# Performance work log

Measured on AMD Instinct MI355X. Metric: run time of the kernel, lower is better.

## Reference

```python
import jax, jax.numpy as jnp
import numpy as np

B, N, C, H = 4, 2048, 1024, 16
D = C // H  # dim_per_head = 64
NEG = -1e9  # stands in for -inf masked_fill (finite to keep grads clean)


def setup_inputs() -> dict:
    key0 = jax.random.key(0)
    ks = jax.random.split(key0, 12)
    inp = {
        "query": jax.random.normal(ks[0], (B, N, C), dtype=jnp.float32),
        "key": jax.random.normal(ks[1], (B, N, C), dtype=jnp.float32),
        "value": jax.random.normal(ks[2], (B, N, C), dtype=jnp.float32),
        "ratio": jax.random.uniform(ks[3], (B, N), dtype=jnp.float32),
        "attn_mask": jax.random.randint(ks[4], (B, N, N), 0, 2) == 1,
        # learned params (Linear layers are bias-free; weights stored as [in, out])
        "Wq": jax.random.normal(ks[5], (C, C), dtype=jnp.float32) / np.sqrt(C),
        "Wk": jax.random.normal(ks[6], (C, C), dtype=jnp.float32) / np.sqrt(C),
        "Wv": jax.random.normal(ks[7], (C, C), dtype=jnp.float32) / np.sqrt(C),
        "Wo": jax.random.normal(ks[8], (C, C), dtype=jnp.float32) / np.sqrt(C),
        "gamma": jnp.ones((C,), dtype=jnp.float32),
        "beta": jnp.zeros((C,), dtype=jnp.float32),
    }
    return inp


def reference(query, key, value, ratio, attn_mask, Wq, Wk, Wv, Wo, gamma, beta):
    residual = query
    # projections -> [B, H, N, D]
    q = (query @ Wq).reshape(B, N, H, D).transpose(0, 2, 1, 3)
    k = (key @ Wk).reshape(B, N, H, D).transpose(0, 2, 1, 3)
    v = (value @ Wv).reshape(B, N, H, D).transpose(0, 2, 1, 3)

    scale = D ** (-0.5)
    scores = jnp.einsum("bhid,bhjd->bhij", q, k) * scale  # [B,H,N1,N2]
    scores = jnp.where(attn_mask[:, None, :, :], NEG, scores)
    scores = scores * ratio[:, None, None, :]  # ratio broadcast over heads & queries
    # NON-STANDARD: softmax over dim=2 (the QUERY axis), faithful to source
    attn = jax.nn.softmax(scores, axis=2)
    # dropout omitted (eval mode)
    ctx = jnp.einsum("bhij,bhjd->bhid", attn, v)  # [B,H,N1,D]
    ctx = ctx.transpose(0, 2, 1, 3).reshape(B, N, C)
    out = ctx @ Wo
    x = residual + out
    # LayerNorm over last dim
    mu = jnp.mean(x, axis=-1, keepdims=True)
    var = jnp.var(x, axis=-1, keepdims=True)
    xn = (x - mu) * jax.lax.rsqrt(var + 1e-5)
    return xn * gamma + beta
```

## Files before the change

### kernel.cpp

```cpp
#include <hip/hip_runtime.h>
#include <hip/hip_bf16.h>
#include <stdint.h>

#define BB 4
#define NN 2048
#define CC 1024
#define HH 16
#define DD 64

typedef __attribute__((ext_vector_type(8))) short bf16x8;
typedef __attribute__((ext_vector_type(4))) float f32x4;

#define LOG2E 1.44269504088896f

__device__ __forceinline__ unsigned short f2bf(float x) {
  uint32_t u = __float_as_uint(x);
  uint32_t r = (u + 0x7FFFu + ((u >> 16) & 1u)) >> 16;
  return (unsigned short)r;
}
__device__ __forceinline__ float bf2f(unsigned short v) {
  return __uint_as_float(((uint32_t)v) << 16);
}
__device__ __forceinline__ float load_in_f(const void* p, size_t idx, int f32in) {
  if (f32in) return ((const float*)p)[idx];
  return bf2f(((const uint16_t*)p)[idx]);
}
__device__ __forceinline__ void gload16(uint16_t* lds_base, const uint16_t* gsrc) {
  __builtin_amdgcn_global_load_lds(
      (const __attribute__((address_space(1))) uint32_t*)(const void*)gsrc,
      (__attribute__((address_space(3))) uint32_t*)(void*)lds_base,
      16, 0, 0);
}

__global__ void detect_kernel(const uint32_t* __restrict__ q,
                              const uint32_t* __restrict__ m,
                              int* __restrict__ flags) {
  if (threadIdx.x == 0 && blockIdx.x == 0) {
    int sane = 0;
    for (int i = 0; i < 128; ++i) {
      uint32_t w = q[i];
      int e0 = (int)((w >> 7) & 0xFFu);
      int e1 = (int)((w >> 23) & 0xFFu);
      sane += (e0 >= 0x70 && e0 <= 0x8F) ? 1 : 0;
      sane += (e1 >= 0x70 && e1 <= 0x8F) ? 1 : 0;
    }
    flags[0] = (sane >= 208) ? 0 : 1;
    int allsmall = 1;
    for (int i = 0; i < 16; ++i) if (m[i] > 1u) allsmall = 0;
    flags[1] = allsmall;
  }
}

__global__ void conv_bf16_3(const void* __restrict__ s0, const void* __restrict__ s1,
                            const void* __restrict__ s2,
                            uint16_t* __restrict__ d0, uint16_t* __restrict__ d1,
                            uint16_t* __restrict__ d2,
                            int n, const int* __restrict__ flags) {
  const int f32in = flags[0];
  const void* src = (blockIdx.z == 0) ? s0 : (blockIdx.z == 1) ? s1 : s2;
  uint16_t* dst = (blockIdx.z == 0) ? d0 : (blockIdx.z == 1) ? d1 : d2;
  int idx = blockIdx.x * blockDim.x + threadIdx.x;
  const int total = n >> 2;
  const int stride = gridDim.x * blockDim.x;
  if (f32in) {
    const float4* s = (const float4*)src;
    for (; idx < total; idx += stride) {
      float4 v = s[idx];
      ushort4 o;
      o.x = f2bf(v.x); o.y = f2bf(v.y); o.z = f2bf(v.z); o.w = f2bf(v.w);
      ((ushort4*)dst)[idx] = o;
    }
  } else {
    const ushort4* s = (const ushort4*)src;
    for (; idx < total; idx += stride) ((ushort4*)dst)[idx] = s[idx];
  }
}

__global__ void conv_ratio2(const void* __restrict__ src, float* __restrict__ rs,
                            float* __restrict__ ng, int n, const int* __restrict__ flags) {
  const int f32in = flags[0];
  int idx = blockIdx.x * blockDim.x + threadIdx.x;
  const int stride = gridDim.x * blockDim.x;
  for (; idx < n; idx += stride) {
    float r = load_in_f(src, idx, f32in);
    rs[idx] = r * 0.125f * LOG2E;
    ng[idx] = r * (-1e9f) * LOG2E;
  }
}

__global__ void conv_maskbits(const void* __restrict__ src, uint32_t* __restrict__ dst,
                              int n, const int* __restrict__ flags) {
  const int isint = flags[1];
  const int gw = (blockIdx.x * blockDim.x + threadIdx.x) >> 6;
  const int lane = threadIdx.x & 63;
  const int nw = (gridDim.x * blockDim.x) >> 6;
  const int totalw = n >> 6;
  for (int w = gw; w < totalw; w += nw) {
    int e = w * 64 + lane;
    bool m;
    if (isint) m = (((const int*)src)[e] != 0);
    else       m = (((const uint8_t*)src)[e] != 0);
    unsigned long long bal = __ballot(m);
    if (lane == 0) ((unsigned long long*)dst)[w] = bal;
  }
}

__global__ __launch_bounds__(256)
void transW(const void* w0, const void* w1, const void* w2, const void* w3,
            uint16_t* __restrict__ wt, const int* __restrict__ flags) {
  const int f32in = flags[0];
  const void* src = (blockIdx.z == 0) ? w0 : (blockIdx.z == 1) ? w1
                   : (blockIdx.z == 2) ? w2 : w3;
  uint16_t* dst = wt + (size_t)blockIdx.z * CC * CC;
  __shared__ float t[32][33];
  const int tx = threadIdx.x, ty = threadIdx.y;
  const int n0 = blockIdx.x * 32, k0 = blockIdx.y * 32;
#pragma unroll
  for (int r = 0; r < 4; ++r) {
    int k = k0 + ty + r * 8;
    t[ty + r * 8][tx] = load_in_f(src, (size_t)k * CC + n0 + tx, f32in);
  }
  __syncthreads();
#pragma unroll
  for (int r = 0; r < 4; ++r) {
    int n = n0 + ty + r * 8;
    dst[(size_t)n * CC + k0 + tx] = f2bf(t[tx][ty + r * 8]);
  }
}

template <int MODE>
__global__ __launch_bounds__(256, 2)
void gemm128(const uint16_t* __restrict__ A, const uint16_t* __restrict__ Bt,
             void* __restrict__ out, const void* __restrict__ resid,
             const float* __restrict__ rowscale, const int* __restrict__ flags) {
  __shared__ uint16_t As[128 * 32];
  __shared__ uint16_t Bs[128 * 32];
  const int tid = threadIdx.x;
  const int wid = tid >> 6, lane = tid & 63;
  const int g = lane >> 4, c = lane & 15;
  const int m0 = blockIdx.x * 128, n0 = blockIdx.y * 128;
  const int wr = wid >> 1, wc = wid & 1;
  f32x4 acc[4][4] = {};
  for (int k0 = 0; k0 < 1024; k0 += 32) {
    __syncthreads();
#pragma unroll
    for (int is = 0; is < 2; ++is) {
      int sb = is * 256 + wid * 64;
      int s = sb + lane;
      int r = s >> 2, kp = s & 3;
      int kps = kp ^ ((r >> 1) & 3);
      gload16(&As[sb * 8], A + (size_t)(m0 + r) * 1024 + k0 + kps * 8);
      gload16(&Bs[sb * 8], Bt + (size_t)(n0 + r) * 1024 + k0 + kps * 8);
    }
    __syncthreads();
    bf16x8 a[4], b[4];
#pragma unroll
    for (int mi = 0; mi < 4; ++mi) {
      int row = wr * 64 + mi * 16 + c;
      a[mi] = *(const bf16x8*)&As[row * 32 + (g ^ ((row >> 1) & 3)) * 8];
    }
#pragma unroll
    for (int ni = 0; ni < 4; ++ni) {
      int row = wc * 64 + ni * 16 + c;
      b[ni] = *(const bf16x8*)&Bs[row * 32 + (g ^ ((row >> 1) & 3)) * 8];
    }
#pragma unroll
    for (int mi = 0; mi < 4; ++mi)
#pragma unroll
      for (int ni = 0; ni < 4; ++ni)
        acc[mi][ni] = __builtin_amdgcn_mfma_f32_16x16x32_bf16(a[mi], b[ni], acc[mi][ni], 0, 0, 0);
  }
  const int f32in = flags[0];
  float rsv[4][4];
  if (MODE == 0 && rowscale) {
#pragma unroll
    for (int mi = 0; mi < 4; ++mi)
#pragma unroll
      for (int r = 0; r < 4; ++r)
        rsv[mi][r] = rowscale[m0 + wr * 64 + mi * 16 + g * 4 + r];
  }
#pragma unroll
  for (int mi = 0; mi < 4; ++mi)
#pragma unroll
    for (int ni = 0; ni < 4; ++ni)
#pragma unroll
      for (int r = 0; r < 4; ++r) {
        int mrow = m0 + wr * 64 + mi * 16 + g * 4 + r;
        int ncol = n0 + wc * 64 + ni * 16 + c;
        float v = acc[mi][ni][r];
        if (MODE == 0) {
          if (rowscale) v *= rsv[mi][r];
          int b_ = mrow >> 11, i = mrow & 2047, h = ncol >> 6, d = ncol & 63;
          ((uint16_t*)out)[((size_t)(b_ * 16 + h) * 2048 + i) * 64 + d] = f2bf(v);
        } else if (MODE == 1) {
          int b_ = mrow >> 11, i = mrow & 2047, h = ncol >> 6, d = ncol & 63;
          ((uint16_t*)out)[((size_t)(b_ * 16 + h) * 64 + d) * 2048 + i] = f2bf(v);
        } else {
          size_t idx = (size_t)mrow * 1024 + ncol;
          ((float*)out)[idx] = v + load_in_f(resid, idx, f32in);
        }
      }
}

__global__ __launch_bounds__(256, 2)
void attn_stats(const uint16_t* __restrict__ qb, const uint16_t* __restrict__ kb,
                uint16_t* __restrict__ vt, const uint32_t* __restrict__ mbits,
                const float* __restrict__ ngbuf) {
  __shared__ float redL[4][128];
  __shared__ float invsh[128];
  const int tid = threadIdx.x, wid = tid >> 6, lane = tid & 63;
  const int g = lane >> 4, c = lane & 15;
  const int bh = blockIdx.x, b_ = bh >> 4;
  const int j0 = blockIdx.y * 128;
  const uint16_t* Kg = kb + (size_t)bh * NN * DD + (size_t)j0 * DD;
  const uint16_t* Qg = qb + (size_t)bh * NN * DD;
  const uint32_t* Mrow = mbits + (size_t)b_ * NN * 64 + (j0 >> 5);
  bf16x8 kf[2][8];
#pragma unroll
  for (int ks = 0; ks < 2; ++ks)
#pragma unroll
    for (int nj = 0; nj < 8; ++nj)
      kf[ks][nj] = *(const bf16x8*)(Kg + (size_t)(nj * 16 + c) * 64 + ks * 32 + g * 8);
  float ng8[8], l_[8];
#pragma unroll
  for (int nj = 0; nj < 8; ++nj) {
    ng8[nj] = ngbuf[b_ * NN + j0 + nj * 16 + c];
    l_[nj] = 0.f;
  }
  bf16x8 qa[2][2], qn[2][2];
  uint4 mqa[8], mqb[8];
#pragma unroll
  for (int ks = 0; ks < 2; ++ks)
#pragma unroll
    for (int mi = 0; mi < 2; ++mi)
      qa[ks][mi] = *(const bf16x8*)(Qg + (size_t)(wid * 32 + mi * 16 + c) * 64 + ks * 32 + g * 8);
#pragma unroll
  for (int u = 0; u < 8; ++u) {
    int mi = u >> 2, r = u & 3;
    mqa[u] = *(const uint4*)(Mrow + (size_t)(wid * 32 + mi * 16 + g * 4 + r) * 64);
  }

  auto body = [&](bf16x8 (&qc)[2][2], bf16x8 (&qp)[2][2],
                  uint4 (&mc)[8], uint4 (&mn)[8], int i0) {
    f32x4 sacc[2][8] = {};
    __builtin_amdgcn_s_setprio(1);
#pragma unroll
    for (int ks = 0; ks < 2; ++ks)
#pragma unroll
      for (int mi = 0; mi < 2; ++mi)
#pragma unroll
        for (int nj = 0; nj < 8; ++nj)
          sacc[mi][nj] = __builtin_amdgcn_mfma_f32_16x16x32_bf16(qc[ks][mi], kf[ks][nj], sacc[mi][nj], 0, 0, 0);
    __builtin_amdgcn_s_setprio(0);
    int ip = (i0 + 128) & (NN - 1);
#pragma unroll
    for (int ks = 0; ks < 2; ++ks)
#pragma unroll
      for (int mi = 0; mi < 2; ++mi)
        qp[ks][mi] = *(const bf16x8*)(Qg + (size_t)(ip + wid * 32 + mi * 16 + c) * 64 + ks * 32 + g * 8);
#pragma unroll
    for (int u = 0; u < 8; ++u) {
      int mi = u >> 2, r = u & 3;
      mn[u] = *(const uint4*)(Mrow + (size_t)(ip + wid * 32 + mi * 16 + g * 4 + r) * 64);
    }
#pragma unroll
    for (int mi = 0; mi < 2; ++mi)
#pragma unroll
      for (int r = 0; r < 4; ++r) {
        const uint4 mw = mc[mi * 4 + r];
#pragma unroll
        for (int nj = 0; nj < 8; ++nj) {
          uint32_t w = (nj < 2) ? mw.x : (nj < 4) ? mw.y : (nj < 6) ? mw.z : mw.w;
          bool bit = (w >> ((nj & 1) * 16 + c)) & 1u;
          float se = bit ? ng8[nj] : sacc[mi][nj][r];
          l_[nj] += exp2f(se);
        }
      }
  };
  for (int it = 0; it < 8; ++it) {
    body(qa, qn, mqa, mqb, it * 256);
    body(qn, qa, mqb, mqa, it * 256 + 128);
  }
#pragma unroll
  for (int nj = 0; nj < 8; ++nj) {
    float l = l_[nj];
    l += __shfl_xor(l, 16);
    l += __shfl_xor(l, 32);
    if (g == 0) redL[wid][nj * 16 + c] = l;
  }
  __syncthreads();
  if (tid < 128) {
    float L = redL[0][tid] + redL[1][tid] + redL[2][tid] + redL[3][tid];
    invsh[tid] = 1.0f / L;
  }
  __syncthreads();
  {
    const int d = tid >> 2, jseg = (tid & 3) * 32;
    uint16_t* vrow = vt + (size_t)bh * DD * NN + (size_t)d * NN + j0 + jseg;
#pragma unroll
    for (int u = 0; u < 4; ++u) {
      bf16x8 v = *(const bf16x8*)(vrow + u * 8);
      bf16x8 o;
#pragma unroll
      for (int e = 0; e < 8; ++e) {
        float f = bf2f((unsigned short)v[e]) * invsh[jseg + u * 8 + e];
        o[e] = (short)f2bf(f);
      }
      *(bf16x8*)(vrow + u * 8) = o;
    }
  }
}

__global__ __launch_bounds__(256, 3)
void attn_pv(const uint16_t* __restrict__ qb, const uint16_t* __restrict__ kb,
             const uint16_t* __restrict__ vt, const uint32_t* __restrict__ mbits,
             const float* __restrict__ ngbuf, uint16_t* __restrict__ ctxr) {
  __shared__ uint16_t Ks[2][64 * 64];
  __shared__ uint16_t Vs[2][64 * 64];
  __shared__ uint16_t Ps[128 * 64];
  const int tid = threadIdx.x, wid = tid >> 6, lane = tid & 63;
  const int g = lane >> 4, c = lane & 15;
  const int bh = blockIdx.x, b_ = bh >> 4, h = bh & 15;
  const int i0 = blockIdx.y * 128;
  const uint16_t* Qg = qb + (size_t)bh * NN * DD;
  const uint16_t* Kg = kb + (size_t)bh * NN * DD;
  const uint16_t* Vg = vt + (size_t)bh * DD * NN;
  const uint32_t* Mb = mbits + (size_t)b_ * NN * 64;
  const float* ngb = ngbuf + b_ * NN;

  auto stageK = [&](int buf, int j0) {
#pragma unroll
    for (int is = 0; is < 2; ++is) {
      int sb = is * 256 + wid * 64;
      int s = sb + lane;
      int row = s >> 3, gr = s & 7;
      gload16(&Ks[buf][sb * 8], Kg + (size_t)(j0 + row) * 64 + (gr ^ (row & 7)) * 8);
    }
  };
  auto stageV = [&](int buf, int j0) {
#pragma unroll
    for (int is = 0; is < 2; ++is) {
      int sb = is * 256 + wid * 64;
      int s = sb + lane;
      int d = s >> 3, gr = s & 7;
      gload16(&Vs[buf][sb * 8], Vg + (size_t)d * NN + j0 + (gr ^ (d & 7)) * 8);
    }
  };

  bf16x8 qf[2][2];
#pragma unroll
  for (int ks = 0; ks < 2; ++ks)
#pragma unroll
    for (int mi = 0; mi < 2; ++mi)
      qf[ks][mi] = *(const bf16x8*)(Qg + (size_t)(i0 + wid * 32 + mi * 16 + c) * 64 + ks * 32 + g * 8);

  stageK(0, 0); stageV(0, 0);
  __syncthreads();

  f32x4 cacc[2][4] = {};
  for (int t = 0; t < 32; ++t) {
    const int j0 = t * 64, cb = t & 1, nb = cb ^ 1;
    if (t < 31) { stageK(nb, j0 + 64); stageV(nb, j0 + 64); }
    uint2 mw0 = *(const uint2*)(Mb + (size_t)(i0 + wid * 32 + c) * 64 + (j0 >> 5));
    uint2 mw1 = *(const uint2*)(Mb + (size_t)(i0 + wid * 32 + 16 + c) * 64 + (j0 >> 5));
    float4 ngv[4];
#pragma unroll
    for (int nj = 0; nj < 4; ++nj)
      ngv[nj] = *(const float4*)(ngb + j0 + nj * 16 + g * 4);
    f32x4 st[4][2] = {};
    __builtin_amdgcn_s_setprio(1);
#pragma unroll
    for (int ks = 0; ks < 2; ++ks) {
      bf16x8 kfr[4];
#pragma unroll
      for (int nj = 0; nj < 4; ++nj) {
        int row = nj * 16 + c;
        kfr[nj] = *(const bf16x8*)&Ks[cb][row * 64 + (((ks * 4 + g) ^ (c & 7))) * 8];
      }
#pragma unroll
      for (int nj = 0; nj < 4; ++nj)
#pragma unroll
        for (int mi = 0; mi < 2; ++mi)
          st[nj][mi] = __builtin_amdgcn_mfma_f32_16x16x32_bf16(kfr[nj], qf[ks][mi], st[nj][mi], 0, 0, 0);
    }
    __builtin_amdgcn_s_setprio(0);
    uint2 pkv[4][2];
#pragma unroll
    for (int nj = 0; nj < 4; ++nj) {
      const float4 ngq = ngv[nj];
      float nz[4] = {ngq.x, ngq.y, ngq.z, ngq.w};
#pragma unroll
      for (int mi = 0; mi < 2; ++mi) {
        const uint2 mw = mi ? mw1 : mw0;
        uint32_t w = (nj < 2) ? mw.x : mw.y;
        float p[4];
#pragma unroll
        for (int u = 0; u < 4; ++u) {
          bool bit = (w >> ((nj & 1) * 16 + g * 4 + u)) & 1u;
          float se = bit ? nz[u] : st[nj][mi][u];
          p[u] = exp2f(se);
        }
        uint32_t lo, hi;
        asm("v_cvt_pk_bf16_f32 %0, %1, %2" : "=v"(lo) : "v"(p[0]), "v"(p[1]));
        asm("v_cvt_pk_bf16_f32 %0, %1, %2" : "=v"(hi) : "v"(p[2]), "v"(p[3]));
        pkv[nj][mi] = make_uint2(lo, hi);
      }
    }
#pragma unroll
    for (int nj = 0; nj < 4; ++nj)
#pragma unroll
      for (int mi = 0; mi < 2; ++mi) {
        int iL = wid * 32 + mi * 16 + c;
        int gran = (nj * 2 + (g >> 1)) ^ (c & 7);
        *(uint2*)((char*)Ps + iL * 128 + gran * 16 + (g & 1) * 8) = pkv[nj][mi];
      }
    __syncthreads();
    __builtin_amdgcn_s_setprio(1);
#pragma unroll
    for (int ks = 0; ks < 2; ++ks) {
      bf16x8 pa[2], vb[4];
#pragma unroll
      for (int mi = 0; mi < 2; ++mi) {
        int row = wid * 32 + mi * 16 + c;
        pa[mi] = *(const bf16x8*)((const char*)Ps + row * 128 + (((ks * 4 + g) ^ (c & 7))) * 16);
      }
#pragma unroll
      for (int nd = 0; nd < 4; ++nd) {
        int row = nd * 16 + c;
        vb[nd] = *(const bf16x8*)&Vs[cb][row * 64 + (((ks * 4 + g) ^ (c & 7))) * 8];
      }
#pragma unroll
      for (int mi = 0; mi < 2; ++mi)
#pragma unroll
        for (int nd = 0; nd < 4; ++nd)
          cacc[mi][nd] = __builtin_amdgcn_mfma_f32_16x16x32_bf16(pa[mi], vb[nd], cacc[mi][nd], 0, 0, 0);
    }
    __builtin_amdgcn_s_setprio(0);
    __syncthreads();
  }
#pragma unroll
  for (int mi = 0; mi < 2; ++mi)
#pragma unroll
    for (int nd = 0; nd < 4; ++nd)
#pragma unroll
      for (int r = 0; r < 4; ++r) {
        int i = i0 + wid * 32 + mi * 16 + g * 4 + r;
        int d = nd * 16 + c;
        ctxr[((size_t)(b_ * NN + i)) * CC + h * DD + d] = f2bf(cacc[mi][nd][r]);
      }
}

__global__ __launch_bounds__(256)
void ln_kernel(const float* __restrict__ xbuf, const void* __restrict__ gamma,
               const void* __restrict__ beta, float* __restrict__ out,
               const int* __restrict__ flags) {
  const int row = blockIdx.x;
  const int tid = threadIdx.x;
  const float4 v = ((const float4*)(xbuf + (size_t)row * CC))[tid];
  float s = v.x + v.y + v.z + v.w;
  float s2 = v.x * v.x + v.y * v.y + v.z * v.z + v.w * v.w;
#pragma unroll
  for (int off = 32; off >= 1; off >>= 1) {
    s += __shfl_xor(s, off);
    s2 += __shfl_xor(s2, off);
  }
  __shared__ float red[8];
  const int wid = tid >> 6, lane = tid & 63;
  if (lane == 0) { red[wid] = s; red[4 + wid] = s2; }
  __syncthreads();
  float ts = red[0] + red[1] + red[2] + red[3];
  float ts2 = red[4] + red[5] + red[6] + red[7];
  float mu = ts * (1.f / 1024.f);
  float var = ts2 * (1.f / 1024.f) - mu * mu;
  float rs = rsqrtf(var + 1e-5f);
  const int f32in = flags[0];
  const int cbase = tid * 4;
  float4 o;
  o.x = (v.x - mu) * rs * load_in_f(gamma, cbase + 0, f32in) + load_in_f(beta, cbase + 0, f32in);
  o.y = (v.y - mu) * rs * load_in_f(gamma, cbase + 1, f32in) + load_in_f(beta, cbase + 1, f32in);
  o.z = (v.z - mu) * rs * load_in_f(gamma, cbase + 2, f32in) + load_in_f(beta, cbase + 2, f32in);
  o.w = (v.w - mu) * rs * load_in_f(gamma, cbase + 3, f32in) + load_in_f(beta, cbase + 3, f32in);
  ((float4*)(out + (size_t)row * CC))[tid] = o;
}

extern "C" void kernel_launch(void* const* d_in, const int* in_sizes, int n_in,
                              void* d_out, int out_size, void* d_ws, size_t ws_size,
                              hipStream_t stream) {
  (void)in_sizes; (void)n_in; (void)out_size; (void)ws_size;
  char* ws = (char*)d_ws;
  size_t off = 0;
  auto alloc = [&](size_t bytes) -> void* {
    void* p = ws + off;
    off += (bytes + 255) & ~(size_t)255;
    return p;
  };
  int*      flags   = (int*)alloc(256);
  float*    rsbuf   = (float*)alloc((size_t)BB * NN * 4);
  float*    ngbuf   = (float*)alloc((size_t)BB * NN * 4);
  uint32_t* mbits   = (uint32_t*)alloc((size_t)BB * NN * 64 * 4);
  uint16_t* xq      = (uint16_t*)alloc((size_t)BB * NN * CC * 2);
  uint16_t* xk      = (uint16_t*)alloc((size_t)BB * NN * CC * 2);
  uint16_t* xv      = (uint16_t*)alloc((size_t)BB * NN * CC * 2);
  uint16_t* qb      = (uint16_t*)alloc((size_t)BB * NN * CC * 2);
  uint16_t* kb      = (uint16_t*)alloc((size_t)BB * NN * CC * 2);
  uint16_t* vtb     = (uint16_t*)alloc((size_t)BB * NN * CC * 2);
  uint16_t* Wt      = (uint16_t*)alloc((size_t)4 * CC * CC * 2);
  uint16_t* ctxr    = xq;
  float*    xbuf    = (float*)xk;

  detect_kernel<<<1, 64, 0, stream>>>((const uint32_t*)d_in[0], (const uint32_t*)d_in[4], flags);
  conv_bf16_3<<<dim3(2048, 1, 3), 256, 0, stream>>>(d_in[0], d_in[1], d_in[2],
                                                    xq, xk, xv, BB * NN * CC, flags);
  conv_ratio2<<<32, 256, 0, stream>>>(d_in[3], rsbuf, ngbuf, BB * NN, flags);
  conv_maskbits<<<2048, 256, 0, stream>>>(d_in[4], mbits, BB * NN * NN, flags);
  transW<<<dim3(32, 32, 4), dim3(32, 8), 0, stream>>>(d_in[5], d_in[6], d_in[7], d_in[8], Wt, flags);

  gemm128<0><<<dim3(64, 8), 256, 0, stream>>>(xq, Wt,               qb,  nullptr, nullptr, flags);
  gemm128<0><<<dim3(64, 8), 256, 0, stream>>>(xk, Wt + 1 * CC * CC, kb,  nullptr, rsbuf,  flags);
  gemm128<1><<<dim3(64, 8), 256, 0, stream>>>(xv, Wt + 2 * CC * CC, vtb, nullptr, nullptr, flags);

  attn_stats<<<dim3(64, 16), 256, 0, stream>>>(qb, kb, vtb, mbits, ngbuf);
  attn_pv<<<dim3(64, 16), 256, 0, stream>>>(qb, kb, vtb, mbits, ngbuf, ctxr);

  gemm128<2><<<dim3(64, 8), 256, 0, stream>>>(ctxr, Wt + 3 * CC * CC, xbuf, d_in[0], nullptr, flags);
  ln_kernel<<<8192, 256, 0, stream>>>(xbuf, d_in[9], d_in[10], (float*)d_out, flags);
}
```

Baseline: 474.1 us.

## Merge QKV projections into one launch and single-buffer V in attn_pv

The three projection GEMMs become one kernel launched on a 64x24 grid. Each block picks its input and weight slice from the column index, so all 1536 tiles can fill the GPU at once instead of 512 per launch. In attn_pv, V goes from a double-buffered to a single shared tile, loaded at the start of each iteration, which cuts LDS so the launch bound can rise from 3 to 4 blocks per SIMD. The trade-off is that the V load is no longer prefetched a tile ahead and must be hidden behind the QK/softmax work, which may add stalls.

```diff
diff --git a/kernel.cpp b/kernel.cpp
--- a/kernel.cpp
+++ b/kernel.cpp
@@ -128,11 +128,85 @@
   }
 }
 
-template <int MODE>
 __global__ __launch_bounds__(256, 2)
-void gemm128(const uint16_t* __restrict__ A, const uint16_t* __restrict__ Bt,
-             void* __restrict__ out, const void* __restrict__ resid,
-             const float* __restrict__ rowscale, const int* __restrict__ flags) {
+void gemmQKV(const uint16_t* __restrict__ xq, const uint16_t* __restrict__ xk,
+             const uint16_t* __restrict__ xv, const uint16_t* __restrict__ Wt,
+             uint16_t* __restrict__ qb, uint16_t* __restrict__ kb,
+             uint16_t* __restrict__ vtb, const float* __restrict__ rowscale) {
+  __shared__ uint16_t As[128 * 32];
+  __shared__ uint16_t Bs[128 * 32];
+  const int tid = threadIdx.x;
+  const int wid = tid >> 6, lane = tid & 63;
+  const int g = lane >> 4, c = lane & 15;
+  const int n0g = blockIdx.y * 128;
+  const int sel = n0g >> 10;
+  const int n0 = n0g & 1023;
+  const int m0 = blockIdx.x * 128;
+  const uint16_t* A = (sel == 0) ? xq : (sel == 1) ? xk : xv;
+  const uint16_t* Bt = Wt + (size_t)sel * CC * CC;
+  const int wr = wid >> 1, wc = wid & 1;
+  f32x4 acc[4][4] = {};
+  for (int k0 = 0; k0 < 1024; k0 += 32) {
+    __syncthreads();
+#pragma unroll
+    for (int is = 0; is < 2; ++is) {
+      int sb = is * 256 + wid * 64;
+      int s = sb + lane;
+      int r = s >> 2, kp = s & 3;
+      int kps = kp ^ ((r >> 1) & 3);
+      gload16(&As[sb * 8], A + (size_t)(m0 + r) * 1024 + k0 + kps * 8);
+      gload16(&Bs[sb * 8], Bt + (size_t)(n0 + r) * 1024 + k0 + kps * 8);
+    }
+    __syncthreads();
+    bf16x8 a[4], b[4];
+#pragma unroll
+    for (int mi = 0; mi < 4; ++mi) {
+      int row = wr * 64 + mi * 16 + c;
+      a[mi] = *(const bf16x8*)&As[row * 32 + (g ^ ((row >> 1) & 3)) * 8];
+    }
+#pragma unroll
+    for (int ni = 0; ni < 4; ++ni) {
+      int row = wc * 64 + ni * 16 + c;
+      b[ni] = *(const bf16x8*)&Bs[row * 32 + (g ^ ((row >> 1) & 3)) * 8];
+    }
+#pragma unroll
+    for (int mi = 0; mi < 4; ++mi)
+#pragma unroll
+      for (int ni = 0; ni < 4; ++ni)
+        acc[mi][ni] = __builtin_amdgcn_mfma_f32_16x16x32_bf16(a[mi], b[ni], acc[mi][ni], 0, 0, 0);
+  }
+  float rsv[4][4];
+  if (sel == 1) {
+#pragma unroll
+    for (int mi = 0; mi < 4; ++mi)
+#pragma unroll
+      for (int r = 0; r < 4; ++r)
+        rsv[mi][r] = rowscale[m0 + wr * 64 + mi * 16 + g * 4 + r];
+  }
+#pragma unroll
+  for (int mi = 0; mi < 4; ++mi)
+#pragma unroll
+    for (int ni = 0; ni < 4; ++ni)
+#pragma unroll
+      for (int r = 0; r < 4; ++r) {
+        int mrow = m0 + wr * 64 + mi * 16 + g * 4 + r;
+        int ncol = n0 + wc * 64 + ni * 16 + c;
+        float v = acc[mi][ni][r];
+        int b_ = mrow >> 11, i = mrow & 2047, h = ncol >> 6, d = ncol & 63;
+        if (sel == 0) {
+          qb[((size_t)(b_ * 16 + h) * 2048 + i) * 64 + d] = f2bf(v);
+        } else if (sel == 1) {
+          kb[((size_t)(b_ * 16 + h) * 2048 + i) * 64 + d] = f2bf(v * rsv[mi][r]);
+        } else {
+          vtb[((size_t)(b_ * 16 + h) * 64 + d) * 2048 + i] = f2bf(v);
+        }
+      }
+}
+
+__global__ __launch_bounds__(256, 2)
+void gemmO(const uint16_t* __restrict__ A, const uint16_t* __restrict__ Bt,
+           float* __restrict__ out, const void* __restrict__ resid,
+           const int* __restrict__ flags) {
   __shared__ uint16_t As[128 * 32];
   __shared__ uint16_t Bs[128 * 32];
   const int tid = threadIdx.x;
@@ -171,14 +245,6 @@
         acc[mi][ni] = __builtin_amdgcn_mfma_f32_16x16x32_bf16(a[mi], b[ni], acc[mi][ni], 0, 0, 0);
   }
   const int f32in = flags[0];
-  float rsv[4][4];
-  if (MODE == 0 && rowscale) {
-#pragma unroll
-    for (int mi = 0; mi < 4; ++mi)
-#pragma unroll
-      for (int r = 0; r < 4; ++r)
-        rsv[mi][r] = rowscale[m0 + wr * 64 + mi * 16 + g * 4 + r];
-  }
 #pragma unroll
   for (int mi = 0; mi < 4; ++mi)
 #pragma unroll
@@ -187,18 +253,8 @@
       for (int r = 0; r < 4; ++r) {
         int mrow = m0 + wr * 64 + mi * 16 + g * 4 + r;
         int ncol = n0 + wc * 64 + ni * 16 + c;
-        float v = acc[mi][ni][r];
-        if (MODE == 0) {
-          if (rowscale) v *= rsv[mi][r];
-          int b_ = mrow >> 11, i = mrow & 2047, h = ncol >> 6, d = ncol & 63;
-          ((uint16_t*)out)[((size_t)(b_ * 16 + h) * 2048 + i) * 64 + d] = f2bf(v);
-        } else if (MODE == 1) {
-          int b_ = mrow >> 11, i = mrow & 2047, h = ncol >> 6, d = ncol & 63;
-          ((uint16_t*)out)[((size_t)(b_ * 16 + h) * 64 + d) * 2048 + i] = f2bf(v);
-        } else {
-          size_t idx = (size_t)mrow * 1024 + ncol;
-          ((float*)out)[idx] = v + load_in_f(resid, idx, f32in);
-        }
+        size_t idx = (size_t)mrow * 1024 + ncol;
+        out[idx] = acc[mi][ni][r] + load_in_f(resid, idx, f32in);
       }
 }
 
@@ -311,12 +367,12 @@
   }
 }
 
-__global__ __launch_bounds__(256, 3)
+__global__ __launch_bounds__(256, 4)
 void attn_pv(const uint16_t* __restrict__ qb, const uint16_t* __restrict__ kb,
              const uint16_t* __restrict__ vt, const uint32_t* __restrict__ mbits,
              const float* __restrict__ ngbuf, uint16_t* __restrict__ ctxr) {
   __shared__ uint16_t Ks[2][64 * 64];
-  __shared__ uint16_t Vs[2][64 * 64];
+  __shared__ uint16_t Vs[64 * 64];
   __shared__ uint16_t Ps[128 * 64];
   const int tid = threadIdx.x, wid = tid >> 6, lane = tid & 63;
   const int g = lane >> 4, c = lane & 15;
@@ -337,13 +393,13 @@
       gload16(&Ks[buf][sb * 8], Kg + (size_t)(j0 + row) * 64 + (gr ^ (row & 7)) * 8);
     }
   };
-  auto stageV = [&](int buf, int j0) {
+  auto stageV = [&](int j0) {
 #pragma unroll
     for (int is = 0; is < 2; ++is) {
       int sb = is * 256 + wid * 64;
       int s = sb + lane;
       int d = s >> 3, gr = s & 7;
-      gload16(&Vs[buf][sb * 8], Vg + (size_t)d * NN + j0 + (gr ^ (d & 7)) * 8);
+      gload16(&Vs[sb * 8], Vg + (size_t)d * NN + j0 + (gr ^ (d & 7)) * 8);
     }
   };
 
@@ -354,13 +410,14 @@
     for (int mi = 0; mi < 2; ++mi)
       qf[ks][mi] = *(const bf16x8*)(Qg + (size_t)(i0 + wid * 32 + mi * 16 + c) * 64 + ks * 32 + g * 8);
 
-  stageK(0, 0); stageV(0, 0);
+  stageK(0, 0);
   __syncthreads();
 
   f32x4 cacc[2][4] = {};
   for (int t = 0; t < 32; ++t) {
     const int j0 = t * 64, cb = t & 1, nb = cb ^ 1;
-    if (t < 31) { stageK(nb, j0 + 64); stageV(nb, j0 + 64); }
+    stageV(j0);
+    if (t < 31) stageK(nb, j0 + 64);
     uint2 mw0 = *(const uint2*)(Mb + (size_t)(i0 + wid * 32 + c) * 64 + (j0 >> 5));
     uint2 mw1 = *(const uint2*)(Mb + (size_t)(i0 + wid * 32 + 16 + c) * 64 + (j0 >> 5));
     float4 ngv[4];
@@ -427,7 +484,7 @@
 #pragma unroll
       for (int nd = 0; nd < 4; ++nd) {
         int row = nd * 16 + c;
-        vb[nd] = *(const bf16x8*)&Vs[cb][row * 64 + (((ks * 4 + g) ^ (c & 7))) * 8];
+        vb[nd] = *(const bf16x8*)&Vs[row * 64 + (((ks * 4 + g) ^ (c & 7))) * 8];
       }
 #pragma unroll
       for (int mi = 0; mi < 2; ++mi)
@@ -515,13 +572,11 @@
   conv_maskbits<<<2048, 256, 0, stream>>>(d_in[4], mbits, BB * NN * NN, flags);
   transW<<<dim3(32, 32, 4), dim3(32, 8), 0, stream>>>(d_in[5], d_in[6], d_in[7], d_in[8], Wt, flags);
 
-  gemm128<0><<<dim3(64, 8), 256, 0, stream>>>(xq, Wt,               qb,  nullptr, nullptr, flags);
-  gemm128<0><<<dim3(64, 8), 256, 0, stream>>>(xk, Wt + 1 * CC * CC, kb,  nullptr, rsbuf,  flags);
-  gemm128<1><<<dim3(64, 8), 256, 0, stream>>>(xv, Wt + 2 * CC * CC, vtb, nullptr, nullptr, flags);
+  gemmQKV<<<dim3(64, 24), 256, 0, stream>>>(xq, xk, xv, Wt, qb, kb, vtb, rsbuf);
 
   attn_stats<<<dim3(64, 16), 256, 0, stream>>>(qb, kb, vtb, mbits, ngbuf);
   attn_pv<<<dim3(64, 16), 256, 0, stream>>>(qb, kb, vtb, mbits, ngbuf, ctxr);
 
-  gemm128<2><<<dim3(64, 8), 256, 0, stream>>>(ctxr, Wt + 3 * CC * CC, xbuf, d_in[0], nullptr, flags);
+  gemmO<<<dim3(64, 8), 256, 0, stream>>>(ctxr, Wt + 3 * CC * CC, xbuf, d_in[0], flags);
   ln_kernel<<<8192, 256, 0, stream>>>(xbuf, d_in[9], d_in[10], (float*)d_out, flags);
 }
```

Result: slower. 563.1 us (+18.8%).
